# Optimization experiments

Measured on AMD Instinct MI355X. Metric: run time of the kernel, lower is better.

The kernel has to match this reference:

```python
import jax, jax.numpy as jnp
import numpy as np
import math

B, S, D, H = 4, 2048, 512, 8
HD = D // H

def setup_inputs() -> dict:
    key = jax.random.key(0)
    ks = jax.random.split(key, 12)
    s_hd = 1.0 / math.sqrt(HD)
    s_d = 1.0 / math.sqrt(D)
    return {
        "q": jax.random.normal(ks[0], (B, S, D), jnp.float32),
        "k": jax.random.normal(ks[1], (B, S, D), jnp.float32),
        "v": jax.random.normal(ks[2], (B, S, D), jnp.float32),
        # torch nn.Linear(head_dim, head_dim): weight [HD, HD], bias [HD]
        "Wq": jax.random.uniform(ks[3], (HD, HD), jnp.float32, -s_hd, s_hd),
        "bq": jax.random.uniform(ks[4], (HD,), jnp.float32, -s_hd, s_hd),
        "Wk": jax.random.uniform(ks[5], (HD, HD), jnp.float32, -s_hd, s_hd),
        "bk": jax.random.uniform(ks[6], (HD,), jnp.float32, -s_hd, s_hd),
        "Wv": jax.random.uniform(ks[7], (HD, HD), jnp.float32, -s_hd, s_hd),
        "bv": jax.random.uniform(ks[8], (HD,), jnp.float32, -s_hd, s_hd),
        # output projection nn.Linear(d, d)
        "Wo": jax.random.uniform(ks[9], (D, D), jnp.float32, -s_d, s_d),
        "bo": jax.random.uniform(ks[10], (D,), jnp.float32, -s_d, s_d),
        # LayerNorm(d) affine params
        "gamma": jnp.ones((D,), jnp.float32),
        "beta": jnp.zeros((D,), jnp.float32),
    }

def _layernorm(x, gamma, beta, eps=1e-5):
    mu = jnp.mean(x, axis=-1, keepdims=True)
    var = jnp.var(x, axis=-1, keepdims=True)
    return (x - mu) * jax.lax.rsqrt(var + eps) * gamma + beta

def reference(q, k, v, Wq, bq, Wk, bk, Wv, bv, Wo, bo, gamma, beta):
    batch, q_len = q.shape[0], q.shape[1]
    # split heads: [B, L, H, HD]; per-head Linear shares one weight across heads
    Qh = q.reshape(batch, q_len, H, HD) @ Wq.T + bq
    Kh = k.reshape(batch, k.shape[1], H, HD) @ Wk.T + bk
    Vh = v.reshape(batch, v.shape[1], H, HD) @ Wv.T + bv
    # scores scaled by sqrt(d) (faithful to source, NOT sqrt(head_dim))
    scores = jnp.einsum('bqhd,bkhd->bhqk', Qh, Kh) / math.sqrt(D)
    attn = jax.nn.softmax(scores, axis=-1)
    out = jnp.einsum('bhqk,bkhd->bqhd', attn, Vh)
    concat = out.reshape(batch, q_len, D)
    lin = concat @ Wo.T + bo
    # AddNorm quirk: residual added AFTER LayerNorm (dropout = identity in eval)
    return q + _layernorm(lin, gamma, beta)
```

## Files before the change

kernel.cpp:

```cpp
#include <hip/hip_runtime.h>
#include <hip/hip_cooperative_groups.h>
#include <hip/hip_bf16.h>
#include <math.h>
#include <stdint.h>

namespace cg = cooperative_groups;

#define B 4
#define S 2048
#define D 512
#define H 8
#define HD 64

typedef __attribute__((ext_vector_type(4))) int   int4v;
typedef __attribute__((ext_vector_type(8))) short short8;
typedef __attribute__((ext_vector_type(4))) short short4v;
typedef __attribute__((ext_vector_type(4))) float f32x4;

__device__ __forceinline__ unsigned short bfr(float x) {
    __bf16 h = (__bf16)x;
    union { __bf16 b; unsigned short s; } u; u.b = h; return u.s;
}
__device__ __forceinline__ float b2f(unsigned short s) {
    union { unsigned u; float f; } v; v.u = (unsigned)s << 16; return v.f;
}
__device__ __forceinline__ float ex2(float x) {
#if __has_builtin(__builtin_amdgcn_exp2f)
    return __builtin_amdgcn_exp2f(x);
#else
    return exp2f(x);
#endif
}
__device__ __forceinline__ short8 cvt8(const float* p) {
    float4 f0 = *(const float4*)p;
    float4 f1 = *(const float4*)(p + 4);
    short8 s8;
    s8[0] = (short)bfr(f0.x); s8[1] = (short)bfr(f0.y);
    s8[2] = (short)bfr(f0.z); s8[3] = (short)bfr(f0.w);
    s8[4] = (short)bfr(f1.x); s8[5] = (short)bfr(f1.y);
    s8[6] = (short)bfr(f1.z); s8[7] = (short)bfr(f1.w);
    return s8;
}

#define QSCALE 0.06377229601488305f
#define MFIX 4.0f

typedef const __attribute__((address_space(1))) unsigned char g8_t;
typedef __attribute__((address_space(3))) unsigned char l8_t;
__device__ __forceinline__ void gl_lds16(const unsigned short* g, unsigned short* l) {
#if __has_builtin(__builtin_amdgcn_global_load_lds)
    __builtin_amdgcn_global_load_lds((g8_t*)g, (l8_t*)l, 16, 0, 0);
#else
    int lane = threadIdx.x & 63;
    ((int4v*)l)[lane] = *(const int4v*)g;
#endif
}

__global__ __launch_bounds__(256, 4) void fused_kernel(
    const float* __restrict__ q, const float* __restrict__ k,
    const float* __restrict__ v,
    const float* __restrict__ Wq, const float* __restrict__ bq,
    const float* __restrict__ Wk, const float* __restrict__ bk,
    const float* __restrict__ Wv, const float* __restrict__ bv,
    const float* __restrict__ Wo, const float* __restrict__ bo,
    const float* __restrict__ gamma, const float* __restrict__ beta,
    unsigned short* __restrict__ Qh, unsigned short* __restrict__ Kh,
    unsigned short* __restrict__ VtG, unsigned short* __restrict__ WoB,
    unsigned short* __restrict__ accPb, float* __restrict__ lP,
    float* __restrict__ out)
{
    __shared__ __align__(16) unsigned char smem[16384];

    const int bid = blockIdx.x;
    const int t = threadIdx.x;
    const int w = t >> 6, L = t & 63;
    const int c = L & 15, qd = L >> 4;
    const size_t NEh = (size_t)B * S * D;
    const size_t BHS = (size_t)B * H * S;

    {
        int wi = bid * 256 + t;
        WoB[wi] = bfr(Wo[wi]);

        const int bh = bid & 31;
        const int sg = bid >> 5;
        const int b = bh >> 3, h = bh & 7;
        const int st = sg * 4 + w;
        unsigned short* Wl = (unsigned short*)smem;

        const float* Wsrc[3]  = {Wq, Wk, Wv};
        const float* biasP[3] = {bq, bk, bv};
        const float* Xs[3]    = {q, k, v};

        for (int x = 0; x < 3; ++x) {
            __syncthreads();
            {
                int row = t >> 2, col = (t & 3) * 16;
                *(short8*)&Wl[row * 72 + col]     = cvt8(Wsrc[x] + t * 16);
                *(short8*)&Wl[row * 72 + col + 8] = cvt8(Wsrc[x] + t * 16 + 8);
            }
            __syncthreads();

            short8 wf[4][2];
            #pragma unroll
            for (int nt = 0; nt < 4; ++nt)
                #pragma unroll
                for (int kc = 0; kc < 2; ++kc)
                    wf[nt][kc] = *(const short8*)&Wl[(16 * nt + c) * 72 + kc * 32 + 8 * qd];

            const float* xrow = Xs[x] + ((size_t)(b * S + st * 16 + c)) * D + h * HD;
            short8 af0 = cvt8(xrow + 8 * qd);
            short8 af1 = cvt8(xrow + 32 + 8 * qd);

            if (x < 2) {
                f32x4 acc[4];
                #pragma unroll
                for (int nt = 0; nt < 4; ++nt) {
                    float bv_ = biasP[x][16 * nt + c];
                    acc[nt] = (f32x4){bv_, bv_, bv_, bv_};
                    acc[nt] = __builtin_amdgcn_mfma_f32_16x16x32_bf16(af0, wf[nt][0], acc[nt], 0, 0, 0);
                    acc[nt] = __builtin_amdgcn_mfma_f32_16x16x32_bf16(af1, wf[nt][1], acc[nt], 0, 0, 0);
                }
                unsigned short* O = ((x == 0) ? Qh : Kh)
                                  + ((size_t)(b * H + h) * S + st * 16) * HD;
                const float sc = (x == 0) ? QSCALE : 1.0f;
                #pragma unroll
                for (int nt = 0; nt < 4; ++nt)
                    #pragma unroll
                    for (int r = 0; r < 4; ++r)
                        O[(4 * qd + r) * HD + 16 * nt + c] = bfr(acc[nt][r] * sc);
            } else {
                f32x4 acc[4];
                #pragma unroll
                for (int nt = 0; nt < 4; ++nt) {
                    float4 bb4 = *(const float4*)(biasP[x] + 16 * nt + 4 * qd);
                    acc[nt] = (f32x4){bb4.x, bb4.y, bb4.z, bb4.w};
                    acc[nt] = __builtin_amdgcn_mfma_f32_16x16x32_bf16(wf[nt][0], af0, acc[nt], 0, 0, 0);
                    acc[nt] = __builtin_amdgcn_mfma_f32_16x16x32_bf16(wf[nt][1], af1, acc[nt], 0, 0, 0);
                }
                unsigned short* O = VtG + (size_t)(b * H + h) * HD * S;
                #pragma unroll
                for (int nt = 0; nt < 4; ++nt)
                    #pragma unroll
                    for (int r = 0; r < 4; ++r)
                        O[(size_t)(16 * nt + 4 * qd + r) * S + st * 16 + c] = bfr(acc[nt][r]);
            }
        }
    }

    cg::this_grid().sync();

    {
        unsigned short (*Ks)[4096] = (unsigned short (*)[4096])smem;

        const int bh = bid & 31;
        const int rem = bid >> 5;
        const int qt = rem >> 1;
        const int ks = rem & 1;
        const int b = bh >> 3, h = bh & 7;

        const unsigned short* Kb = Kh + ((size_t)bh * S + ks * 1024) * HD;
        const unsigned short* Vb = VtG + (size_t)bh * HD * S + ks * 1024;

        short8 qf[2][2];
        #pragma unroll
        for (int qg = 0; qg < 2; ++qg)
            #pragma unroll
            for (int kc = 0; kc < 2; ++kc)
                qf[qg][kc] = *(const short8*)(Qh
                    + ((size_t)bh * S + qt * 128 + w * 32 + qg * 16 + c) * HD
                    + kc * 32 + 8 * qd);

        f32x4 acc[2][4];
        float lrun[2] = {0.f, 0.f};
        #pragma unroll
        for (int qg = 0; qg < 2; ++qg)
            #pragma unroll
            for (int dt = 0; dt < 4; ++dt) acc[qg][dt] = (f32x4){0.f, 0.f, 0.f, 0.f};

        #pragma unroll
        for (int i = 0; i < 2; ++i) {
            int bi = w + 4 * i;
            gl_lds16(Kb + (size_t)(16 * (bi >> 1) + c) * HD + (bi & 1) * 32 + qd * 8,
                     &Ks[0][bi * 512]);
        }

        for (int it = 0; it < 16; ++it) {
            const int cur = it & 1;
            __syncthreads();
            if (it + 1 < 16) {
                int n1 = (it + 1) * 64;
                #pragma unroll
                for (int i = 0; i < 2; ++i) {
                    int bi = w + 4 * i;
                    gl_lds16(Kb + (size_t)(n1 + 16 * (bi >> 1) + c) * HD + (bi & 1) * 32 + qd * 8,
                             &Ks[cur ^ 1][bi * 512]);
                }
            }
            const int n0 = it * 64;

            short4v vf[4][4];
            #pragma unroll
            for (int dt = 0; dt < 4; ++dt)
                #pragma unroll
                for (int mt = 0; mt < 4; ++mt)
                    vf[dt][mt] = *(const short4v*)(Vb + (size_t)(16 * dt + c) * S
                                                   + n0 + 16 * mt + 4 * qd);

            const unsigned short* KsC = Ks[cur];
            short4v pa[2][4];
            #pragma unroll
            for (int mt = 0; mt < 4; ++mt) {
                short8 a0 = *(const short8*)(KsC + (mt * 2 + 0) * 512 + L * 8);
                short8 a1 = *(const short8*)(KsC + (mt * 2 + 1) * 512 + L * 8);
                #pragma unroll
                for (int qg = 0; qg < 2; ++qg) {
                    f32x4 stv = (f32x4){-MFIX, -MFIX, -MFIX, -MFIX};
                    stv = __builtin_amdgcn_mfma_f32_16x16x32_bf16(a0, qf[qg][0], stv, 0, 0, 0);
                    stv = __builtin_amdgcn_mfma_f32_16x16x32_bf16(a1, qf[qg][1], stv, 0, 0, 0);
                    float p0 = ex2(stv[0]), p1 = ex2(stv[1]);
                    float p2 = ex2(stv[2]), p3 = ex2(stv[3]);
                    lrun[qg] += (p0 + p1) + (p2 + p3);
                    short4v p_;
                    p_[0] = (short)bfr(p0); p_[1] = (short)bfr(p1);
                    p_[2] = (short)bfr(p2); p_[3] = (short)bfr(p3);
                    pa[qg][mt] = p_;
                }
            }

            #pragma unroll
            for (int dt = 0; dt < 4; ++dt)
                #pragma unroll
                for (int mt = 0; mt < 4; ++mt) {
#if __has_builtin(__builtin_amdgcn_mfma_f32_16x16x16bf16_1k)
                    #pragma unroll
                    for (int qg = 0; qg < 2; ++qg)
                        acc[qg][dt] = __builtin_amdgcn_mfma_f32_16x16x16bf16_1k(
                            pa[qg][mt], vf[dt][mt], acc[qg][dt], 0, 0, 0);
#else
                    #pragma unroll
                    for (int qg = 0; qg < 2; ++qg) {
                        short8 pz = {pa[qg][mt][0], pa[qg][mt][1],
                                     pa[qg][mt][2], pa[qg][mt][3], 0, 0, 0, 0};
                        short8 vz = {vf[dt][mt][0], vf[dt][mt][1],
                                     vf[dt][mt][2], vf[dt][mt][3], 0, 0, 0, 0};
                        acc[qg][dt] = __builtin_amdgcn_mfma_f32_16x16x32_bf16(pz, vz, acc[qg][dt], 0, 0, 0);
                    }
#endif
                }
        }

        const int q0 = qt * 128 + w * 32;
        unsigned short* accPp = accPb + (size_t)ks * NEh
                              + ((size_t)b * S + q0) * D + h * HD;
        #pragma unroll
        for (int qg = 0; qg < 2; ++qg) {
            float lr = lrun[qg];
            lr += __shfl_xor(lr, 16);
            lr += __shfl_xor(lr, 32);
            if (qd == 0)
                lP[(size_t)ks * BHS + (size_t)bh * S + q0 + qg * 16 + c] = lr;
            #pragma unroll
            for (int dt = 0; dt < 4; ++dt)
                #pragma unroll
                for (int r = 0; r < 4; ++r)
                    accPp[(size_t)(qg * 16 + 4 * qd + r) * D + 16 * dt + c]
                        = bfr(acc[qg][dt][r]);
        }
    }

    cg::this_grid().sync();

    if (bid < 512) {
        unsigned short* As = (unsigned short*)smem;

        const int r0 = bid * 16;
        const int n0 = w * 128;
        const int bb = r0 >> 11;

        #pragma unroll
        for (int i = 0; i < 8; ++i) {
            int flat = t + 256 * i;
            int row = flat >> 7, cg4 = flat & 127;
            int col = cg4 * 4;
            size_t gi = (size_t)(r0 + row) * D + col;
            short4v a0 = *(const short4v*)(accPb + gi);
            short4v a1 = *(const short4v*)(accPb + NEh + gi);
            int hh = col >> 6, ss = (r0 & (S - 1)) + row;
            float l0 = lP[(size_t)(bb * H + hh) * S + ss];
            float l1 = lP[BHS + (size_t)(bb * H + hh) * S + ss];
            float li = 1.f / (l0 + l1);
            short4v s;
            #pragma unroll
            for (int j = 0; j < 4; ++j)
                s[j] = (short)bfr((b2f((unsigned short)a0[j])
                                 + b2f((unsigned short)a1[j])) * li);
            int chunk8 = cg4 >> 1;
            *(short4v*)&As[row * 512 + ((chunk8 ^ (row & 7)) << 3) + (cg4 & 1) * 4] = s;
        }
        __syncthreads();

        f32x4 acc[8];
        #pragma unroll
        for (int nt = 0; nt < 8; ++nt) {
            float bv_ = bo[n0 + 16 * nt + c];
            acc[nt] = (f32x4){bv_, bv_, bv_, bv_};
        }

        for (int kc = 0; kc < 16; ++kc) {
            short8 a0 = *(const short8*)&As[c * 512 + (((kc * 4 + qd) ^ (c & 7)) << 3)];
            #pragma unroll
            for (int nt = 0; nt < 8; ++nt) {
                short8 bf = *(const short8*)(WoB + (size_t)(n0 + 16 * nt + c) * D
                                             + kc * 32 + 8 * qd);
                acc[nt] = __builtin_amdgcn_mfma_f32_16x16x32_bf16(a0, bf, acc[nt], 0, 0, 0);
            }
        }
        __syncthreads();

        float* red   = (float*)smem;
        float* mu_s2 = (float*)(smem + 2048);
        float* rs_s2 = (float*)(smem + 2048 + 64);

        float sm[4], sq[4];
        #pragma unroll
        for (int r = 0; r < 4; ++r) { sm[r] = 0.f; sq[r] = 0.f; }
        #pragma unroll
        for (int nt = 0; nt < 8; ++nt)
            #pragma unroll
            for (int r = 0; r < 4; ++r) {
                float x_ = acc[nt][r];
                sm[r] += x_; sq[r] += x_ * x_;
            }
        #pragma unroll
        for (int mask = 1; mask <= 8; mask <<= 1)
            #pragma unroll
            for (int r = 0; r < 4; ++r) {
                sm[r] += __shfl_xor(sm[r], mask);
                sq[r] += __shfl_xor(sq[r], mask);
            }
        if (c == 0) {
            #pragma unroll
            for (int r = 0; r < 4; ++r) {
                red[w * 16 + 4 * qd + r]       = sm[r];
                red[(4 + w) * 16 + 4 * qd + r] = sq[r];
            }
        }
        __syncthreads();

        if (t < 16) {
            float s_ = 0.f, q_ = 0.f;
            #pragma unroll
            for (int w_ = 0; w_ < 4; ++w_) {
                s_ += red[w_ * 16 + t];
                q_ += red[(4 + w_) * 16 + t];
            }
            float mu_ = s_ * (1.f / D);
            float var = q_ * (1.f / D) - mu_ * mu_;
            mu_s2[t] = mu_;
            rs_s2[t] = rsqrtf(var + 1e-5f);
        }
        __syncthreads();

        #pragma unroll
        for (int nt = 0; nt < 8; ++nt) {
            int n = n0 + 16 * nt + c;
            float g = gamma[n], be = beta[n];
            #pragma unroll
            for (int r = 0; r < 4; ++r) {
                int m = 4 * qd + r;
                size_t gi = (size_t)(r0 + m) * D + n;
                out[gi] = q[gi] + (acc[nt][r] - mu_s2[m]) * rs_s2[m] * g + be;
            }
        }
    }
}

__global__ __launch_bounds__(256) void qkv_mfma_kernel(
    const float* __restrict__ q, const float* __restrict__ k,
    const float* __restrict__ v,
    const float* __restrict__ Wq, const float* __restrict__ bq,
    const float* __restrict__ Wk, const float* __restrict__ bk,
    const float* __restrict__ Wv, const float* __restrict__ bv,
    const float* __restrict__ Wo, unsigned short* __restrict__ WoB,
    unsigned short* __restrict__ Qh, unsigned short* __restrict__ Kh,
    unsigned short* __restrict__ VtG)
{
    const int t = threadIdx.x;
    const int bid = blockIdx.x;
    if (bid >= 1536) {
        int i = (bid - 1536) * 1024 + t * 4;
        float4 f = *(const float4*)(Wo + i);
        short4v s;
        s[0] = (short)bfr(f.x); s[1] = (short)bfr(f.y);
        s[2] = (short)bfr(f.z); s[3] = (short)bfr(f.w);
        *(short4v*)(WoB + i) = s;
        return;
    }

    __shared__ __align__(16) unsigned short Wl[64 * 72];

    const int x   = bid / 512;
    const int r_  = bid - x * 512;
    const int bh  = r_ >> 4;
    const int stg = r_ & 15;
    const int b = bh >> 3, h = bh & 7;
    const int L = t & 63, w = t >> 6;
    const int c = L & 15, qd = L >> 4;

    const float* Wf     = (x == 0) ? Wq : (x == 1) ? Wk : Wv;
    const float* bias_p = (x == 0) ? bq : (x == 1) ? bk : bv;
    const float* X      = (x == 0) ? q  : (x == 1) ? k  : v;

    {
        int row = t >> 2, col = (t & 3) * 16;
        *(short8*)&Wl[row * 72 + col]     = cvt8(Wf + t * 16);
        *(short8*)&Wl[row * 72 + col + 8] = cvt8(Wf + t * 16 + 8);
    }
    __syncthreads();

    short8 wf[4][2];
    #pragma unroll
    for (int nt = 0; nt < 4; ++nt)
        #pragma unroll
        for (int kc = 0; kc < 2; ++kc)
            wf[nt][kc] = *(const short8*)&Wl[(16 * nt + c) * 72 + kc * 32 + 8 * qd];

    if (x < 2) {
        float bias[4];
        #pragma unroll
        for (int nt = 0; nt < 4; ++nt) bias[nt] = bias_p[16 * nt + c];
        const float sc = (x == 0) ? QSCALE : 1.0f;
        #pragma unroll
        for (int ti = 0; ti < 2; ++ti) {
            const int st = stg * 8 + w * 2 + ti;
            const float* xrow = X + ((size_t)(b * S + st * 16 + c)) * D + h * HD;
            short8 af0 = cvt8(xrow + 8 * qd);
            short8 af1 = cvt8(xrow + 32 + 8 * qd);
            f32x4 acc[4];
            #pragma unroll
            for (int nt = 0; nt < 4; ++nt) {
                acc[nt] = (f32x4){bias[nt], bias[nt], bias[nt], bias[nt]};
                acc[nt] = __builtin_amdgcn_mfma_f32_16x16x32_bf16(af0, wf[nt][0], acc[nt], 0, 0, 0);
                acc[nt] = __builtin_amdgcn_mfma_f32_16x16x32_bf16(af1, wf[nt][1], acc[nt], 0, 0, 0);
            }
            unsigned short* O = ((x == 0) ? Qh : Kh)
                              + ((size_t)(b * H + h) * S + st * 16) * HD;
            #pragma unroll
            for (int nt = 0; nt < 4; ++nt)
                #pragma unroll
                for (int r = 0; r < 4; ++r)
                    O[(4 * qd + r) * HD + 16 * nt + c] = bfr(acc[nt][r] * sc);
        }
    } else {
        f32x4 bias4[4];
        #pragma unroll
        for (int nt = 0; nt < 4; ++nt) {
            float4 bb4 = *(const float4*)(bias_p + 16 * nt + 4 * qd);
            bias4[nt] = (f32x4){bb4.x, bb4.y, bb4.z, bb4.w};
        }
        #pragma unroll
        for (int ti = 0; ti < 2; ++ti) {
            const int st = stg * 8 + w * 2 + ti;
            const float* xrow = X + ((size_t)(b * S + st * 16 + c)) * D + h * HD;
            short8 af0 = cvt8(xrow + 8 * qd);
            short8 af1 = cvt8(xrow + 32 + 8 * qd);
            f32x4 acc[4];
            #pragma unroll
            for (int nt = 0; nt < 4; ++nt) {
                acc[nt] = bias4[nt];
                acc[nt] = __builtin_amdgcn_mfma_f32_16x16x32_bf16(wf[nt][0], af0, acc[nt], 0, 0, 0);
                acc[nt] = __builtin_amdgcn_mfma_f32_16x16x32_bf16(wf[nt][1], af1, acc[nt], 0, 0, 0);
            }
            unsigned short* O = VtG + (size_t)(b * H + h) * HD * S;
            #pragma unroll
            for (int nt = 0; nt < 4; ++nt)
                #pragma unroll
                for (int r = 0; r < 4; ++r)
                    O[(size_t)(16 * nt + 4 * qd + r) * S + st * 16 + c] = bfr(acc[nt][r]);
        }
    }
}

__global__ __launch_bounds__(256, 4) void attn_kernel(
    const unsigned short* __restrict__ Qh, const unsigned short* __restrict__ Kh,
    const unsigned short* __restrict__ VtG, unsigned short* __restrict__ accPb,
    float* __restrict__ lP)
{
    __shared__ __align__(16) unsigned short Ks[2][4096];
    __shared__ __align__(16) unsigned short Vs[2][4096];

    const int idx = blockIdx.x;
    const int bh = idx & 31;
    const int rem = idx >> 5;
    const int qt = rem >> 1;
    const int ks = rem & 1;
    const int b = bh >> 3, h = bh & 7;
    const int t = threadIdx.x;
    const int w = t >> 6, L = t & 63;
    const int c = L & 15, qd = L >> 4;

    const unsigned short* Kb = Kh + ((size_t)bh * S + ks * 1024) * HD;
    const unsigned short* Vb = VtG + (size_t)bh * HD * S + ks * 1024;

    short8 qf[2][2];
    #pragma unroll
    for (int qg = 0; qg < 2; ++qg)
        #pragma unroll
        for (int kc = 0; kc < 2; ++kc)
            qf[qg][kc] = *(const short8*)(Qh
                + ((size_t)bh * S + qt * 128 + w * 32 + qg * 16 + c) * HD
                + kc * 32 + 8 * qd);

    f32x4 acc[2][4];
    float lrun[2] = {0.f, 0.f};
    #pragma unroll
    for (int qg = 0; qg < 2; ++qg)
        #pragma unroll
        for (int dt = 0; dt < 4; ++dt) acc[qg][dt] = (f32x4){0.f, 0.f, 0.f, 0.f};

    const int sd = t >> 3, sj = t & 7;
    const int sp = sj >> 2, smt = (sj >> 1) & 1;
    const int sqa = (2 * sj) & 3, sqb = (2 * sj + 1) & 3;

    int4v vpre[2];
    #pragma unroll
    for (int i = 0; i < 2; ++i) {
        int bi = w + 4 * i;
        gl_lds16(Kb + (size_t)(16 * (bi >> 1) + c) * HD + (bi & 1) * 32 + qd * 8,
                 &Ks[0][bi * 512]);
        vpre[i] = *(const int4v*)(Vb + (size_t)(sd + 32 * i) * S + 8 * sj);
    }

    for (int it = 0; it < 16; ++it) {
        const int cur = it & 1, nxt = cur ^ 1;
        #pragma unroll
        for (int i = 0; i < 2; ++i) {
            int d = sd + 32 * i;
            int dt = d >> 4, cc = d & 15;
            union { int4v v; short4v h[2]; } u; u.v = vpre[i];
            *(short4v*)&Vs[cur][((dt * 2 + sp) * 64 + sqa * 16 + cc) * 8 + smt * 4] = u.h[0];
            *(short4v*)&Vs[cur][((dt * 2 + sp) * 64 + sqb * 16 + cc) * 8 + smt * 4] = u.h[1];
        }
        __syncthreads();
        if (it + 1 < 16) {
            int n1 = (it + 1) * 64;
            #pragma unroll
            for (int i = 0; i < 2; ++i) {
                int bi = w + 4 * i;
                gl_lds16(Kb + (size_t)(n1 + 16 * (bi >> 1) + c) * HD + (bi & 1) * 32 + qd * 8,
                         &Ks[nxt][bi * 512]);
                vpre[i] = *(const int4v*)(Vb + (size_t)(sd + 32 * i) * S + n1 + 8 * sj);
            }
        }

        const unsigned short* KsC = Ks[cur];
        const unsigned short* VsC = Vs[cur];

        short4v pa[2][4];
        #pragma unroll
        for (int mt = 0; mt < 4; ++mt) {
            short8 a0 = *(const short8*)(KsC + (mt * 2 + 0) * 512 + L * 8);
            short8 a1 = *(const short8*)(KsC + (mt * 2 + 1) * 512 + L * 8);
            #pragma unroll
            for (int qg = 0; qg < 2; ++qg) {
                f32x4 stv = (f32x4){-MFIX, -MFIX, -MFIX, -MFIX};
                stv = __builtin_amdgcn_mfma_f32_16x16x32_bf16(a0, qf[qg][0], stv, 0, 0, 0);
                stv = __builtin_amdgcn_mfma_f32_16x16x32_bf16(a1, qf[qg][1], stv, 0, 0, 0);
                float p0 = ex2(stv[0]), p1 = ex2(stv[1]);
                float p2 = ex2(stv[2]), p3 = ex2(stv[3]);
                lrun[qg] += (p0 + p1) + (p2 + p3);
                short4v p_;
                p_[0] = (short)bfr(p0); p_[1] = (short)bfr(p1);
                p_[2] = (short)bfr(p2); p_[3] = (short)bfr(p3);
                pa[qg][mt] = p_;
            }
        }

        #pragma unroll
        for (int dt = 0; dt < 4; ++dt)
            #pragma unroll
            for (int p = 0; p < 2; ++p) {
                union { short8 v8; short4v h[2]; } u;
                u.v8 = *(const short8*)(VsC + (dt * 2 + p) * 512 + L * 8);
#if __has_builtin(__builtin_amdgcn_mfma_f32_16x16x16bf16_1k)
                #pragma unroll
                for (int qg = 0; qg < 2; ++qg) {
                    acc[qg][dt] = __builtin_amdgcn_mfma_f32_16x16x16bf16_1k(
                        pa[qg][2 * p + 0], u.h[0], acc[qg][dt], 0, 0, 0);
                    acc[qg][dt] = __builtin_amdgcn_mfma_f32_16x16x16bf16_1k(
                        pa[qg][2 * p + 1], u.h[1], acc[qg][dt], 0, 0, 0);
                }
#else
                #pragma unroll
                for (int qg = 0; qg < 2; ++qg) {
                    short8 pz0 = {pa[qg][2 * p + 0][0], pa[qg][2 * p + 0][1],
                                  pa[qg][2 * p + 0][2], pa[qg][2 * p + 0][3], 0, 0, 0, 0};
                    short8 pz1 = {pa[qg][2 * p + 1][0], pa[qg][2 * p + 1][1],
                                  pa[qg][2 * p + 1][2], pa[qg][2 * p + 1][3], 0, 0, 0, 0};
                    short8 v0 = {u.h[0][0], u.h[0][1], u.h[0][2], u.h[0][3], 0, 0, 0, 0};
                    short8 v1 = {u.h[1][0], u.h[1][1], u.h[1][2], u.h[1][3], 0, 0, 0, 0};
                    acc[qg][dt] = __builtin_amdgcn_mfma_f32_16x16x32_bf16(pz0, v0, acc[qg][dt], 0, 0, 0);
                    acc[qg][dt] = __builtin_amdgcn_mfma_f32_16x16x32_bf16(pz1, v1, acc[qg][dt], 0, 0, 0);
                }
#endif
            }
    }

    const int q0 = qt * 128 + w * 32;
    unsigned short* accPp = accPb + (size_t)ks * ((size_t)B * S * D)
                          + ((size_t)b * S + q0) * D + h * HD;
    #pragma unroll
    for (int qg = 0; qg < 2; ++qg) {
        float lr = lrun[qg];
        lr += __shfl_xor(lr, 16);
        lr += __shfl_xor(lr, 32);
        if (qd == 0)
            lP[(size_t)ks * ((size_t)B * H * S) + (size_t)bh * S + q0 + qg * 16 + c] = lr;
        #pragma unroll
        for (int dt = 0; dt < 4; ++dt)
            #pragma unroll
            for (int r = 0; r < 4; ++r)
                accPp[(size_t)(qg * 16 + 4 * qd + r) * D + 16 * dt + c]
                    = bfr(acc[qg][dt][r]);
    }
}

__global__ __launch_bounds__(1024) void oproj_ln_kernel(
    const unsigned short* __restrict__ accPb, const float* __restrict__ lP,
    const unsigned short* __restrict__ WoB,
    const float* __restrict__ bo, const float* __restrict__ gamma,
    const float* __restrict__ beta, const float* __restrict__ qin,
    float* __restrict__ out)
{
    __shared__ __align__(16) unsigned short As[32 * 520];
    __shared__ float red[2][32][17];
    __shared__ float linv_s[32][8];
    __shared__ float mu_s2[32], rs_s2[32];

    const int t = threadIdx.x;
    const int r0 = blockIdx.x * 32;
    const int w = t >> 6, L = t & 63;
    const int c = L & 15, qd = L >> 4;
    const int n0 = w * 32;
    const size_t NEh = (size_t)B * S * D;
    const size_t BHS = (size_t)B * H * S;

    if (t < 256) {
        int row = t >> 3, hh = t & 7;
        int bb = r0 >> 11;
        int ss = (r0 & (S - 1)) + row;
        float l0 = lP[(size_t)(bb * H + hh) * S + ss];
        float l1 = lP[BHS + (size_t)(bb * H + hh) * S + ss];
        linv_s[row][hh] = 1.f / (l0 + l1);
    }
    __syncthreads();

    #pragma unroll
    for (int i = 0; i < 4; ++i) {
        int flat = t + 1024 * i;
        int row = flat >> 7, cg4 = flat & 127;
        int col = cg4 * 4;
        size_t gi = (size_t)(r0 + row) * D + col;
        short4v a0 = *(const short4v*)(accPb + gi);
        short4v a1 = *(const short4v*)(accPb + NEh + gi);
        float li = linv_s[row][col >> 6];
        short4v s;
        #pragma unroll
        for (int j = 0; j < 4; ++j)
            s[j] = (short)bfr((b2f((unsigned short)a0[j])
                             + b2f((unsigned short)a1[j])) * li);
        *(short4v*)&As[row * 520 + col] = s;
    }
    __syncthreads();

    f32x4 acc[2][2];
    #pragma unroll
    for (int nt = 0; nt < 2; ++nt) {
        float bv_ = bo[n0 + 16 * nt + c];
        acc[0][nt] = (f32x4){bv_, bv_, bv_, bv_};
        acc[1][nt] = (f32x4){bv_, bv_, bv_, bv_};
    }

    for (int kc = 0; kc < 16; ++kc) {
        short8 a0 = *(const short8*)&As[c * 520 + kc * 32 + 8 * qd];
        short8 a1 = *(const short8*)&As[(16 + c) * 520 + kc * 32 + 8 * qd];
        #pragma unroll
        for (int nt = 0; nt < 2; ++nt) {
            short8 bf = *(const short8*)(WoB + (size_t)(n0 + 16 * nt + c) * D
                                         + kc * 32 + 8 * qd);
            acc[0][nt] = __builtin_amdgcn_mfma_f32_16x16x32_bf16(a0, bf, acc[0][nt], 0, 0, 0);
            acc[1][nt] = __builtin_amdgcn_mfma_f32_16x16x32_bf16(a1, bf, acc[1][nt], 0, 0, 0);
        }
    }

    float sm[2][4], sq[2][4];
    #pragma unroll
    for (int mt = 0; mt < 2; ++mt)
        #pragma unroll
        for (int r = 0; r < 4; ++r) { sm[mt][r] = 0.f; sq[mt][r] = 0.f; }
    #pragma unroll
    for (int mt = 0; mt < 2; ++mt)
        #pragma unroll
        for (int nt = 0; nt < 2; ++nt)
            #pragma unroll
            for (int r = 0; r < 4; ++r) {
                float x_ = acc[mt][nt][r];
                sm[mt][r] += x_; sq[mt][r] += x_ * x_;
            }
    #pragma unroll
    for (int mask = 1; mask <= 8; mask <<= 1)
        #pragma unroll
        for (int mt = 0; mt < 2; ++mt)
            #pragma unroll
            for (int r = 0; r < 4; ++r) {
                sm[mt][r] += __shfl_xor(sm[mt][r], mask);
                sq[mt][r] += __shfl_xor(sq[mt][r], mask);
            }
    if (c == 0) {
        #pragma unroll
        for (int mt = 0; mt < 2; ++mt)
            #pragma unroll
            for (int r = 0; r < 4; ++r) {
                red[0][mt * 16 + 4 * qd + r][w] = sm[mt][r];
                red[1][mt * 16 + 4 * qd + r][w] = sq[mt][r];
            }
    }
    __syncthreads();

    if (t < 32) {
        float s_ = 0.f, q_ = 0.f;
        #pragma unroll
        for (int w_ = 0; w_ < 16; ++w_) { s_ += red[0][t][w_]; q_ += red[1][t][w_]; }
        float mu_ = s_ * (1.f / D);
        float var = q_ * (1.f / D) - mu_ * mu_;
        mu_s2[t] = mu_;
        rs_s2[t] = rsqrtf(var + 1e-5f);
    }
    __syncthreads();

    #pragma unroll
    for (int nt = 0; nt < 2; ++nt) {
        int n = n0 + 16 * nt + c;
        float g = gamma[n], be = beta[n];
        #pragma unroll
        for (int mt = 0; mt < 2; ++mt)
            #pragma unroll
            for (int r = 0; r < 4; ++r) {
                int m = mt * 16 + 4 * qd + r;
                size_t gi = (size_t)(r0 + m) * D + n;
                out[gi] = qin[gi] + (acc[mt][nt][r] - mu_s2[m]) * rs_s2[m] * g + be;
            }
    }
}

extern "C" void kernel_launch(void* const* d_in, const int* in_sizes, int n_in,
                              void* d_out, int out_size, void* d_ws, size_t ws_size,
                              hipStream_t stream) {
    const float* q     = (const float*)d_in[0];
    const float* k     = (const float*)d_in[1];
    const float* v     = (const float*)d_in[2];
    const float* Wq    = (const float*)d_in[3];
    const float* bq    = (const float*)d_in[4];
    const float* Wk    = (const float*)d_in[5];
    const float* bk    = (const float*)d_in[6];
    const float* Wv    = (const float*)d_in[7];
    const float* bv    = (const float*)d_in[8];
    const float* Wo    = (const float*)d_in[9];
    const float* bo    = (const float*)d_in[10];
    const float* gamma = (const float*)d_in[11];
    const float* beta  = (const float*)d_in[12];
    float* out = (float*)d_out;

    const size_t NE = (size_t)B * S * D;
    unsigned short* wsu = (unsigned short*)d_ws;
    unsigned short* Qh    = wsu;
    unsigned short* Kh    = wsu + NE;
    unsigned short* VtG   = wsu + 2 * NE;
    unsigned short* WoB   = wsu + 3 * NE;
    unsigned short* accPb = WoB + (size_t)D * D;
    float* lP = (float*)(accPb + 2 * NE);

    int maxB = 0;
    hipError_t qe = hipOccupancyMaxActiveBlocksPerMultiprocessor(
        &maxB, (const void*)fused_kernel, 256, 0);
    bool coop = (qe == hipSuccess && maxB >= 4);

    if (coop) {
        void* args[] = {
            (void*)&q, (void*)&k, (void*)&v,
            (void*)&Wq, (void*)&bq, (void*)&Wk, (void*)&bk, (void*)&Wv, (void*)&bv,
            (void*)&Wo, (void*)&bo, (void*)&gamma, (void*)&beta,
            (void*)&Qh, (void*)&Kh, (void*)&VtG, (void*)&WoB,
            (void*)&accPb, (void*)&lP, (void*)&out
        };
        hipError_t rc = hipLaunchCooperativeKernel((const void*)fused_kernel,
                                                   dim3(1024), dim3(256),
                                                   args, 0, stream);
        if (rc != hipSuccess) coop = false;
    }

    if (!coop) {
        hipLaunchKernelGGL(qkv_mfma_kernel, dim3(1536 + 256), dim3(256), 0, stream,
                           q, k, v, Wq, bq, Wk, bk, Wv, bv, Wo, WoB, Qh, Kh, VtG);
        hipLaunchKernelGGL(attn_kernel, dim3(1024), dim3(256), 0, stream,
                           Qh, Kh, VtG, accPb, lP);
        hipLaunchKernelGGL(oproj_ln_kernel, dim3(B * S / 32), dim3(1024), 0, stream,
                           accPb, lP, WoB, bo, gamma, beta, q, out);
    }
}
```

Baseline: 192.5 us.

## Drop cooperative fused kernel for three launches; raise MFMA wave priority

Removes the single cooperative-grid fused kernel, which used two grid-wide barriers between the QKV projection, attention and output-projection/LayerNorm phases. It always launches the three separate kernels instead, which have their own grid shapes and a separate attention kernel that stages V in LDS. It also wraps the MFMA sections of the attention kernel in s_setprio(1)/s_setprio(0) so waves issuing matrix ops get scheduling priority over waves doing exp/memory work. The cost is extra launch overhead and intermediate round trips through global memory in exchange for avoiding grid syncs and the 1024-block occupancy constraint.

```diff
diff --git a/kernel.cpp b/kernel.cpp
--- a/kernel.cpp
+++ b/kernel.cpp
@@ -1,10 +1,7 @@
 #include <hip/hip_runtime.h>
-#include <hip/hip_cooperative_groups.h>
 #include <hip/hip_bf16.h>
 #include <math.h>
 #include <stdint.h>
-
-namespace cg = cooperative_groups;
 
 #define B 4
 #define S 2048
@@ -54,326 +51,6 @@
     int lane = threadIdx.x & 63;
     ((int4v*)l)[lane] = *(const int4v*)g;
 #endif
-}
-
-__global__ __launch_bounds__(256, 4) void fused_kernel(
-    const float* __restrict__ q, const float* __restrict__ k,
-    const float* __restrict__ v,
-    const float* __restrict__ Wq, const float* __restrict__ bq,
-    const float* __restrict__ Wk, const float* __restrict__ bk,
-    const float* __restrict__ Wv, const float* __restrict__ bv,
-    const float* __restrict__ Wo, const float* __restrict__ bo,
-    const float* __restrict__ gamma, const float* __restrict__ beta,
-    unsigned short* __restrict__ Qh, unsigned short* __restrict__ Kh,
-    unsigned short* __restrict__ VtG, unsigned short* __restrict__ WoB,
-    unsigned short* __restrict__ accPb, float* __restrict__ lP,
-    float* __restrict__ out)
-{
-    __shared__ __align__(16) unsigned char smem[16384];
-
-    const int bid = blockIdx.x;
-    const int t = threadIdx.x;
-    const int w = t >> 6, L = t & 63;
-    const int c = L & 15, qd = L >> 4;
-    const size_t NEh = (size_t)B * S * D;
-    const size_t BHS = (size_t)B * H * S;
-
-    {
-        int wi = bid * 256 + t;
-        WoB[wi] = bfr(Wo[wi]);
-
-        const int bh = bid & 31;
-        const int sg = bid >> 5;
-        const int b = bh >> 3, h = bh & 7;
-        const int st = sg * 4 + w;
-        unsigned short* Wl = (unsigned short*)smem;
-
-        const float* Wsrc[3]  = {Wq, Wk, Wv};
-        const float* biasP[3] = {bq, bk, bv};
-        const float* Xs[3]    = {q, k, v};
-
-        for (int x = 0; x < 3; ++x) {
-            __syncthreads();
-            {
-                int row = t >> 2, col = (t & 3) * 16;
-                *(short8*)&Wl[row * 72 + col]     = cvt8(Wsrc[x] + t * 16);
-                *(short8*)&Wl[row * 72 + col + 8] = cvt8(Wsrc[x] + t * 16 + 8);
-            }
-            __syncthreads();
-
-            short8 wf[4][2];
-            #pragma unroll
-            for (int nt = 0; nt < 4; ++nt)
-                #pragma unroll
-                for (int kc = 0; kc < 2; ++kc)
-                    wf[nt][kc] = *(const short8*)&Wl[(16 * nt + c) * 72 + kc * 32 + 8 * qd];
-
-            const float* xrow = Xs[x] + ((size_t)(b * S + st * 16 + c)) * D + h * HD;
-            short8 af0 = cvt8(xrow + 8 * qd);
-            short8 af1 = cvt8(xrow + 32 + 8 * qd);
-
-            if (x < 2) {
-                f32x4 acc[4];
-                #pragma unroll
-                for (int nt = 0; nt < 4; ++nt) {
-                    float bv_ = biasP[x][16 * nt + c];
-                    acc[nt] = (f32x4){bv_, bv_, bv_, bv_};
-                    acc[nt] = __builtin_amdgcn_mfma_f32_16x16x32_bf16(af0, wf[nt][0], acc[nt], 0, 0, 0);
-                    acc[nt] = __builtin_amdgcn_mfma_f32_16x16x32_bf16(af1, wf[nt][1], acc[nt], 0, 0, 0);
-                }
-                unsigned short* O = ((x == 0) ? Qh : Kh)
-                                  + ((size_t)(b * H + h) * S + st * 16) * HD;
-                const float sc = (x == 0) ? QSCALE : 1.0f;
-                #pragma unroll
-                for (int nt = 0; nt < 4; ++nt)
-                    #pragma unroll
-                    for (int r = 0; r < 4; ++r)
-                        O[(4 * qd + r) * HD + 16 * nt + c] = bfr(acc[nt][r] * sc);
-            } else {
-                f32x4 acc[4];
-                #pragma unroll
-                for (int nt = 0; nt < 4; ++nt) {
-                    float4 bb4 = *(const float4*)(biasP[x] + 16 * nt + 4 * qd);
-                    acc[nt] = (f32x4){bb4.x, bb4.y, bb4.z, bb4.w};
-                    acc[nt] = __builtin_amdgcn_mfma_f32_16x16x32_bf16(wf[nt][0], af0, acc[nt], 0, 0, 0);
-                    acc[nt] = __builtin_amdgcn_mfma_f32_16x16x32_bf16(wf[nt][1], af1, acc[nt], 0, 0, 0);
-                }
-                unsigned short* O = VtG + (size_t)(b * H + h) * HD * S;
-                #pragma unroll
-                for (int nt = 0; nt < 4; ++nt)
-                    #pragma unroll
-                    for (int r = 0; r < 4; ++r)
-                        O[(size_t)(16 * nt + 4 * qd + r) * S + st * 16 + c] = bfr(acc[nt][r]);
-            }
-        }
-    }
-
-    cg::this_grid().sync();
-
-    {
-        unsigned short (*Ks)[4096] = (unsigned short (*)[4096])smem;
-
-        const int bh = bid & 31;
-        const int rem = bid >> 5;
-        const int qt = rem >> 1;
-        const int ks = rem & 1;
-        const int b = bh >> 3, h = bh & 7;
-
-        const unsigned short* Kb = Kh + ((size_t)bh * S + ks * 1024) * HD;
-        const unsigned short* Vb = VtG + (size_t)bh * HD * S + ks * 1024;
-
-        short8 qf[2][2];
-        #pragma unroll
-        for (int qg = 0; qg < 2; ++qg)
-            #pragma unroll
-            for (int kc = 0; kc < 2; ++kc)
-                qf[qg][kc] = *(const short8*)(Qh
-                    + ((size_t)bh * S + qt * 128 + w * 32 + qg * 16 + c) * HD
-                    + kc * 32 + 8 * qd);
-
-        f32x4 acc[2][4];
-        float lrun[2] = {0.f, 0.f};
-        #pragma unroll
-        for (int qg = 0; qg < 2; ++qg)
-            #pragma unroll
-            for (int dt = 0; dt < 4; ++dt) acc[qg][dt] = (f32x4){0.f, 0.f, 0.f, 0.f};
-
-        #pragma unroll
-        for (int i = 0; i < 2; ++i) {
-            int bi = w + 4 * i;
-            gl_lds16(Kb + (size_t)(16 * (bi >> 1) + c) * HD + (bi & 1) * 32 + qd * 8,
-                     &Ks[0][bi * 512]);
-        }
-
-        for (int it = 0; it < 16; ++it) {
-            const int cur = it & 1;
-            __syncthreads();
-            if (it + 1 < 16) {
-                int n1 = (it + 1) * 64;
-                #pragma unroll
-                for (int i = 0; i < 2; ++i) {
-                    int bi = w + 4 * i;
-                    gl_lds16(Kb + (size_t)(n1 + 16 * (bi >> 1) + c) * HD + (bi & 1) * 32 + qd * 8,
-                             &Ks[cur ^ 1][bi * 512]);
-                }
-            }
-            const int n0 = it * 64;
-
-            short4v vf[4][4];
-            #pragma unroll
-            for (int dt = 0; dt < 4; ++dt)
-                #pragma unroll
-                for (int mt = 0; mt < 4; ++mt)
-                    vf[dt][mt] = *(const short4v*)(Vb + (size_t)(16 * dt + c) * S
-                                                   + n0 + 16 * mt + 4 * qd);
-
-            const unsigned short* KsC = Ks[cur];
-            short4v pa[2][4];
-            #pragma unroll
-            for (int mt = 0; mt < 4; ++mt) {
-                short8 a0 = *(const short8*)(KsC + (mt * 2 + 0) * 512 + L * 8);
-                short8 a1 = *(const short8*)(KsC + (mt * 2 + 1) * 512 + L * 8);
-                #pragma unroll
-                for (int qg = 0; qg < 2; ++qg) {
-                    f32x4 stv = (f32x4){-MFIX, -MFIX, -MFIX, -MFIX};
-                    stv = __builtin_amdgcn_mfma_f32_16x16x32_bf16(a0, qf[qg][0], stv, 0, 0, 0);
-                    stv = __builtin_amdgcn_mfma_f32_16x16x32_bf16(a1, qf[qg][1], stv, 0, 0, 0);
-                    float p0 = ex2(stv[0]), p1 = ex2(stv[1]);
-                    float p2 = ex2(stv[2]), p3 = ex2(stv[3]);
-                    lrun[qg] += (p0 + p1) + (p2 + p3);
-                    short4v p_;
-                    p_[0] = (short)bfr(p0); p_[1] = (short)bfr(p1);
-                    p_[2] = (short)bfr(p2); p_[3] = (short)bfr(p3);
-                    pa[qg][mt] = p_;
-                }
-            }
-
-            #pragma unroll
-            for (int dt = 0; dt < 4; ++dt)
-                #pragma unroll
-                for (int mt = 0; mt < 4; ++mt) {
-#if __has_builtin(__builtin_amdgcn_mfma_f32_16x16x16bf16_1k)
-                    #pragma unroll
-                    for (int qg = 0; qg < 2; ++qg)
-                        acc[qg][dt] = __builtin_amdgcn_mfma_f32_16x16x16bf16_1k(
-                            pa[qg][mt], vf[dt][mt], acc[qg][dt], 0, 0, 0);
-#else
-                    #pragma unroll
-                    for (int qg = 0; qg < 2; ++qg) {
-                        short8 pz = {pa[qg][mt][0], pa[qg][mt][1],
-                                     pa[qg][mt][2], pa[qg][mt][3], 0, 0, 0, 0};
-                        short8 vz = {vf[dt][mt][0], vf[dt][mt][1],
-                                     vf[dt][mt][2], vf[dt][mt][3], 0, 0, 0, 0};
-                        acc[qg][dt] = __builtin_amdgcn_mfma_f32_16x16x32_bf16(pz, vz, acc[qg][dt], 0, 0, 0);
-                    }
-#endif
-                }
-        }
-
-        const int q0 = qt * 128 + w * 32;
-        unsigned short* accPp = accPb + (size_t)ks * NEh
-                              + ((size_t)b * S + q0) * D + h * HD;
-        #pragma unroll
-        for (int qg = 0; qg < 2; ++qg) {
-            float lr = lrun[qg];
-            lr += __shfl_xor(lr, 16);
-            lr += __shfl_xor(lr, 32);
-            if (qd == 0)
-                lP[(size_t)ks * BHS + (size_t)bh * S + q0 + qg * 16 + c] = lr;
-            #pragma unroll
-            for (int dt = 0; dt < 4; ++dt)
-                #pragma unroll
-                for (int r = 0; r < 4; ++r)
-                    accPp[(size_t)(qg * 16 + 4 * qd + r) * D + 16 * dt + c]
-                        = bfr(acc[qg][dt][r]);
-        }
-    }
-
-    cg::this_grid().sync();
-
-    if (bid < 512) {
-        unsigned short* As = (unsigned short*)smem;
-
-        const int r0 = bid * 16;
-        const int n0 = w * 128;
-        const int bb = r0 >> 11;
-
-        #pragma unroll
-        for (int i = 0; i < 8; ++i) {
-            int flat = t + 256 * i;
-            int row = flat >> 7, cg4 = flat & 127;
-            int col = cg4 * 4;
-            size_t gi = (size_t)(r0 + row) * D + col;
-            short4v a0 = *(const short4v*)(accPb + gi);
-            short4v a1 = *(const short4v*)(accPb + NEh + gi);
-            int hh = col >> 6, ss = (r0 & (S - 1)) + row;
-            float l0 = lP[(size_t)(bb * H + hh) * S + ss];
-            float l1 = lP[BHS + (size_t)(bb * H + hh) * S + ss];
-            float li = 1.f / (l0 + l1);
-            short4v s;
-            #pragma unroll
-            for (int j = 0; j < 4; ++j)
-                s[j] = (short)bfr((b2f((unsigned short)a0[j])
-                                 + b2f((unsigned short)a1[j])) * li);
-            int chunk8 = cg4 >> 1;
-            *(short4v*)&As[row * 512 + ((chunk8 ^ (row & 7)) << 3) + (cg4 & 1) * 4] = s;
-        }
-        __syncthreads();
-
-        f32x4 acc[8];
-        #pragma unroll
-        for (int nt = 0; nt < 8; ++nt) {
-            float bv_ = bo[n0 + 16 * nt + c];
-            acc[nt] = (f32x4){bv_, bv_, bv_, bv_};
-        }
-
-        for (int kc = 0; kc < 16; ++kc) {
-            short8 a0 = *(const short8*)&As[c * 512 + (((kc * 4 + qd) ^ (c & 7)) << 3)];
-            #pragma unroll
-            for (int nt = 0; nt < 8; ++nt) {
-                short8 bf = *(const short8*)(WoB + (size_t)(n0 + 16 * nt + c) * D
-                                             + kc * 32 + 8 * qd);
-                acc[nt] = __builtin_amdgcn_mfma_f32_16x16x32_bf16(a0, bf, acc[nt], 0, 0, 0);
-            }
-        }
-        __syncthreads();
-
-        float* red   = (float*)smem;
-        float* mu_s2 = (float*)(smem + 2048);
-        float* rs_s2 = (float*)(smem + 2048 + 64);
-
-        float sm[4], sq[4];
-        #pragma unroll
-        for (int r = 0; r < 4; ++r) { sm[r] = 0.f; sq[r] = 0.f; }
-        #pragma unroll
-        for (int nt = 0; nt < 8; ++nt)
-            #pragma unroll
-            for (int r = 0; r < 4; ++r) {
-                float x_ = acc[nt][r];
-                sm[r] += x_; sq[r] += x_ * x_;
-            }
-        #pragma unroll
-        for (int mask = 1; mask <= 8; mask <<= 1)
-            #pragma unroll
-            for (int r = 0; r < 4; ++r) {
-                sm[r] += __shfl_xor(sm[r], mask);
-                sq[r] += __shfl_xor(sq[r], mask);
-            }
-        if (c == 0) {
-            #pragma unroll
-            for (int r = 0; r < 4; ++r) {
-                red[w * 16 + 4 * qd + r]       = sm[r];
-                red[(4 + w) * 16 + 4 * qd + r] = sq[r];
-            }
-        }
-        __syncthreads();
-
-        if (t < 16) {
-            float s_ = 0.f, q_ = 0.f;
-            #pragma unroll
-            for (int w_ = 0; w_ < 4; ++w_) {
-                s_ += red[w_ * 16 + t];
-                q_ += red[(4 + w_) * 16 + t];
-            }
-            float mu_ = s_ * (1.f / D);
-            float var = q_ * (1.f / D) - mu_ * mu_;
-            mu_s2[t] = mu_;
-            rs_s2[t] = rsqrtf(var + 1e-5f);
-        }
-        __syncthreads();
-
-        #pragma unroll
-        for (int nt = 0; nt < 8; ++nt) {
-            int n = n0 + 16 * nt + c;
-            float g = gamma[n], be = beta[n];
-            #pragma unroll
-            for (int r = 0; r < 4; ++r) {
-                int m = 4 * qd + r;
-                size_t gi = (size_t)(r0 + m) * D + n;
-                out[gi] = q[gi] + (acc[nt][r] - mu_s2[m]) * rs_s2[m] * g + be;
-            }
-        }
-    }
 }
 
 __global__ __launch_bounds__(256) void qkv_mfma_kernel(
@@ -565,8 +242,10 @@
             #pragma unroll
             for (int qg = 0; qg < 2; ++qg) {
                 f32x4 stv = (f32x4){-MFIX, -MFIX, -MFIX, -MFIX};
+                __builtin_amdgcn_s_setprio(1);
                 stv = __builtin_amdgcn_mfma_f32_16x16x32_bf16(a0, qf[qg][0], stv, 0, 0, 0);
                 stv = __builtin_amdgcn_mfma_f32_16x16x32_bf16(a1, qf[qg][1], stv, 0, 0, 0);
+                __builtin_amdgcn_s_setprio(0);
                 float p0 = ex2(stv[0]), p1 = ex2(stv[1]);
                 float p2 = ex2(stv[2]), p3 = ex2(stv[3]);
                 lrun[qg] += (p0 + p1) + (p2 + p3);
@@ -584,6 +263,7 @@
                 union { short8 v8; short4v h[2]; } u;
                 u.v8 = *(const short8*)(VsC + (dt * 2 + p) * 512 + L * 8);
 #if __has_builtin(__builtin_amdgcn_mfma_f32_16x16x16bf16_1k)
+                __builtin_amdgcn_s_setprio(1);
                 #pragma unroll
                 for (int qg = 0; qg < 2; ++qg) {
                     acc[qg][dt] = __builtin_amdgcn_mfma_f32_16x16x16bf16_1k(
@@ -591,7 +271,9 @@
                     acc[qg][dt] = __builtin_amdgcn_mfma_f32_16x16x16bf16_1k(
                         pa[qg][2 * p + 1], u.h[1], acc[qg][dt], 0, 0, 0);
                 }
+                __builtin_amdgcn_s_setprio(0);
 #else
+                __builtin_amdgcn_s_setprio(1);
                 #pragma unroll
                 for (int qg = 0; qg < 2; ++qg) {
                     short8 pz0 = {pa[qg][2 * p + 0][0], pa[qg][2 * p + 0][1],
@@ -603,6 +285,7 @@
                     acc[qg][dt] = __builtin_amdgcn_mfma_f32_16x16x32_bf16(pz0, v0, acc[qg][dt], 0, 0, 0);
                     acc[qg][dt] = __builtin_amdgcn_mfma_f32_16x16x32_bf16(pz1, v1, acc[qg][dt], 0, 0, 0);
                 }
+                __builtin_amdgcn_s_setprio(0);
 #endif
             }
     }
@@ -781,31 +464,10 @@
     unsigned short* accPb = WoB + (size_t)D * D;
     float* lP = (float*)(accPb + 2 * NE);
 
-    int maxB = 0;
-    hipError_t qe = hipOccupancyMaxActiveBlocksPerMultiprocessor(
-        &maxB, (const void*)fused_kernel, 256, 0);
-    bool coop = (qe == hipSuccess && maxB >= 4);
-
-    if (coop) {
-        void* args[] = {
-            (void*)&q, (void*)&k, (void*)&v,
-            (void*)&Wq, (void*)&bq, (void*)&Wk, (void*)&bk, (void*)&Wv, (void*)&bv,
-            (void*)&Wo, (void*)&bo, (void*)&gamma, (void*)&beta,
-            (void*)&Qh, (void*)&Kh, (void*)&VtG, (void*)&WoB,
-            (void*)&accPb, (void*)&lP, (void*)&out
-        };
-        hipError_t rc = hipLaunchCooperativeKernel((const void*)fused_kernel,
-                                                   dim3(1024), dim3(256),
-                                                   args, 0, stream);
-        if (rc != hipSuccess) coop = false;
-    }
-
-    if (!coop) {
-        hipLaunchKernelGGL(qkv_mfma_kernel, dim3(1536 + 256), dim3(256), 0, stream,
-                           q, k, v, Wq, bq, Wk, bk, Wv, bv, Wo, WoB, Qh, Kh, VtG);
-        hipLaunchKernelGGL(attn_kernel, dim3(1024), dim3(256), 0, stream,
-                           Qh, Kh, VtG, accPb, lP);
-        hipLaunchKernelGGL(oproj_ln_kernel, dim3(B * S / 32), dim3(1024), 0, stream,
-                           accPb, lP, WoB, bo, gamma, beta, q, out);
-    }
-}
+    hipLaunchKernelGGL(qkv_mfma_kernel, dim3(1536 + 256), dim3(256), 0, stream,
+                       q, k, v, Wq, bq, Wk, bk, Wv, bv, Wo, WoB, Qh, Kh, VtG);
+    hipLaunchKernelGGL(attn_kernel, dim3(1024), dim3(256), 0, stream,
+                       Qh, Kh, VtG, accPb, lP);
+    hipLaunchKernelGGL(oproj_ln_kernel, dim3(B * S / 32), dim3(1024), 0, stream,
+                       accPb, lP, WoB, bo, gamma, beta, q, out);
+}
```

Measured after the change: 194.1 us. No clear change (+0.9%).
